# Kernel tuning notes

Measured on AMD Instinct MI355X. Metric: run time of the kernel, lower is better.

Reference implementation:

```python
import jax, jax.numpy as jnp
import numpy as np
from jax import lax

B, H, W, C = 2, 96, 96, 96
D_STATE, D_CONV, EXPAND = 16, 3, 2
D_INNER = EXPAND * C            # 192 (VSSBlock inner width)
DM = D_INNER                    # Mamba d_model; Mamba expand=1 -> mamba d_inner == DM
DT_RANK = -(-DM // 16)          # ceil(192/16) = 12


def setup_inputs() -> dict:
    key = jax.random.key(0)
    ks = jax.random.split(key, 12)
    s = lambda k, shp, sc=0.02: jax.random.normal(k, shp, jnp.float32) * sc
    return {
        "x": jax.random.normal(ks[0], (B, H, W, C), jnp.float32),
        "norm_w": jnp.ones((C,), jnp.float32),
        "norm_b": jnp.zeros((C,), jnp.float32),
        "in_proj_w": s(ks[1], (C, 2 * D_INNER)),
        "conv2d_w": s(ks[2], (D_INNER, 1, D_CONV, D_CONV), 0.1),   # depthwise OIHW
        "m_in_proj_w": s(ks[3], (DM, 2 * DM)),
        "m_conv1d_w": s(ks[4], (DM, 1, D_CONV), 0.1),              # depthwise causal OIL
        "m_conv1d_b": jnp.zeros((DM,), jnp.float32),
        "m_x_proj_w": s(ks[5], (DM, DT_RANK + 2 * D_STATE)),
        "m_dt_proj_w": s(ks[6], (DT_RANK, DM), 0.1),
        "m_dt_proj_b": s(ks[7], (DM,), 0.1),
        "m_A_log": jnp.log(jnp.broadcast_to(
            jnp.arange(1, D_STATE + 1, dtype=jnp.float32), (DM, D_STATE))),
        "m_D": jnp.ones((DM,), jnp.float32),
        "m_out_proj_w": s(ks[8], (DM, DM)),
        "out_proj_w": s(ks[9], (D_INNER, C)),
    }


def _layernorm(x, w, b, eps=1e-5):
    mu = x.mean(-1, keepdims=True)
    var = jnp.mean(jnp.square(x - mu), -1, keepdims=True)
    return (x - mu) * lax.rsqrt(var + eps) * w + b


def _selective_scan(u, delta, A, Bm, Cm, Dv):
    # u, delta: (B,L,D); A: (D,N); Bm, Cm: (B,L,N); Dv: (D,)
    dA = jnp.exp(jnp.einsum('bld,dn->bldn', delta, A))           # (B,L,D,N)
    dBu = jnp.einsum('bld,bln->bldn', delta * u, Bm)             # (B,L,D,N)

    def step(h, inp):
        dA_t, dBu_t, C_t = inp
        h = dA_t * h + dBu_t                                      # (B,D,N)
        y = jnp.einsum('bdn,bn->bd', h, C_t)
        return h, y

    h0 = jnp.zeros((u.shape[0], A.shape[0], A.shape[1]), u.dtype)
    xs = (dA.transpose(1, 0, 2, 3), dBu.transpose(1, 0, 2, 3), Cm.transpose(1, 0, 2))
    _, ys = lax.scan(step, h0, xs)
    return ys.transpose(1, 0, 2) + u * Dv                         # (B,L,D)


def _mamba(seq, m_in_proj_w, m_conv1d_w, m_conv1d_b, m_x_proj_w,
           m_dt_proj_w, m_dt_proj_b, m_A_log, m_D, m_out_proj_w):
    # seq: (B,L,DM)
    xm, z = jnp.split(seq @ m_in_proj_w, 2, axis=-1)
    # causal depthwise conv1d over L
    xc = lax.conv_general_dilated(
        jnp.transpose(xm, (0, 2, 1)), m_conv1d_w, (1,), [(D_CONV - 1, 0)],
        feature_group_count=DM, dimension_numbers=('NCH', 'OIH', 'NCH'))
    xm = jax.nn.silu(jnp.transpose(xc + m_conv1d_b[None, :, None], (0, 2, 1)))
    x_dbl = xm @ m_x_proj_w
    dt, Bm, Cm = jnp.split(x_dbl, [DT_RANK, DT_RANK + D_STATE], axis=-1)
    delta = jax.nn.softplus(dt @ m_dt_proj_w + m_dt_proj_b)
    A = -jnp.exp(m_A_log)
    y = _selective_scan(xm, delta, A, Bm, Cm, m_D)
    return (y * jax.nn.silu(z)) @ m_out_proj_w


def reference(x, norm_w, norm_b, in_proj_w, conv2d_w, m_in_proj_w, m_conv1d_w,
              m_conv1d_b, m_x_proj_w, m_dt_proj_w, m_dt_proj_b, m_A_log, m_D,
              m_out_proj_w, out_proj_w):
    Bsz, Hh, Ww, _ = x.shape
    xn = _layernorm(x, norm_w, norm_b)
    x_in, x_gate = jnp.split(xn @ in_proj_w, 2, axis=-1)          # (B,H,W,D_INNER) x2
    # depthwise 3x3 conv, 'same' padding
    xc = lax.conv_general_dilated(
        jnp.transpose(x_in, (0, 3, 1, 2)), conv2d_w, (1, 1), [(1, 1), (1, 1)],
        feature_group_count=D_INNER, dimension_numbers=('NCHW', 'OIHW', 'NCHW'))
    xc = jax.nn.silu(jnp.transpose(xc, (0, 2, 3, 1)))
    seq = xc.reshape(Bsz, Hh * Ww, D_INNER)
    y = _mamba(seq, m_in_proj_w, m_conv1d_w, m_conv1d_b, m_x_proj_w,
               m_dt_proj_w, m_dt_proj_b, m_A_log, m_D, m_out_proj_w)
    y = y.reshape(Bsz, Hh, Ww, D_INNER) * jax.nn.silu(x_gate)
    return x + y @ out_proj_w
```

## Files before the change

kernel.cpp:

```cpp
#include <hip/hip_runtime.h>

#define DEV_INLINE __device__ __forceinline__

constexpr int BATCH = 2;
constexpr int HH = 96, WW = 96, CC = 96;
constexpr int DI = 192;
constexpr int NS = 16;
constexpr int LSEQ = HH * WW;
constexpr int TT = BATCH * LSEQ;
constexpr int CHUNK = 32;
constexpr int NCHUNK = LSEQ / CHUNK;
constexpr int QDN = DI * NS;

typedef __attribute__((ext_vector_type(8))) short bf16x8;
typedef __attribute__((ext_vector_type(4))) float f32x4;

DEV_INLINE float silu_f(float x) { return x / (1.f + __expf(-x)); }
DEV_INLINE float softplus_f(float x) {
  return fmaxf(x, 0.f) + log1pf(__expf(-fabsf(x)));
}
DEV_INLINE ushort f2bf(float f) {
  union { float f; unsigned u; } c; c.f = f;
  unsigned u = c.u + 0x7FFF + ((c.u >> 16) & 1);
  return (ushort)(u >> 16);
}
DEV_INLINE float bf2f(ushort u) {
  union { unsigned u; float f; } c; c.u = ((unsigned)u) << 16; return c.f;
}

__global__ __launch_bounds__(256)
void castw_kernel(const float* __restrict__ w0, const float* __restrict__ w1,
                  const float* __restrict__ w2, const float* __restrict__ w3,
                  const float* __restrict__ wx, const float* __restrict__ wdt,
                  const float* __restrict__ wc1,
                  ushort* __restrict__ t0, ushort* __restrict__ t1,
                  ushort* __restrict__ t2, ushort* __restrict__ t3,
                  ushort* __restrict__ t4, ushort* __restrict__ t5,
                  float* __restrict__ cwT)
{
  int id = blockIdx.x * 256 + threadIdx.x;
  if (id < 36864) {
    int k = id % 96, n = id / 96;
    t0[id] = f2bf(w0[k * 384 + n]);
  } else if (id < 110592) {
    int j = id - 36864; int k = j % 192, n = j / 192;
    t1[j] = f2bf(w1[k * 384 + n]);
  } else if (id < 147456) {
    int j = id - 110592; int k = j % 192, n = j / 192;
    t2[j] = f2bf(w2[k * 192 + n]);
  } else if (id < 172032) {
    int j = id - 147456; int k = j % 192, n = j / 192;
    t3[j] = (n < 96) ? f2bf(w3[k * 96 + n]) : (ushort)0;
  } else if (id < 181248) {
    int j = id - 172032; int k = j % 192, n = j / 192;
    float v = 0.f;
    if (n < 16) v = wx[k * 44 + 12 + n];
    else if (n < 32) v = wx[k * 44 + 28 + (n - 16)];
    else if (n < 44) v = wx[k * 44 + (n - 32)];
    t4[j] = f2bf(v);
  } else if (id < 187392) {
    int j = id - 181248; int r = j % 32, d = j / 32;
    t5[j] = (r < 12) ? f2bf(wdt[r * 192 + d]) : (ushort)0;
  } else if (id < 187968) {
    int j = id - 187392; int k = j / 192, d = j % 192;
    cwT[j] = wc1[d * 3 + k];
  }
}

__global__ __launch_bounds__(256)
void ln_inproj_kernel(const float* __restrict__ x, const float* __restrict__ nw,
                      const float* __restrict__ nbias, const ushort* __restrict__ Wt0,
                      ushort* __restrict__ xz0)
{
  __shared__ ushort sA[128][104];
  const int tid = threadIdx.x;
  const int m0 = blockIdx.x * 128;
  const int n0 = blockIdx.y * 64;
  {
    const int tok = tid >> 1, h = tid & 1;
    const float* xr = x + (size_t)(m0 + tok) * 96 + h * 48;
    float v[48];
    float s = 0.f, ss = 0.f;
#pragma unroll
    for (int i = 0; i < 12; ++i) {
      float4 t4 = *(const float4*)(xr + i * 4);
      v[i*4+0] = t4.x; v[i*4+1] = t4.y; v[i*4+2] = t4.z; v[i*4+3] = t4.w;
      s += (t4.x + t4.y) + (t4.z + t4.w);
      ss += (t4.x*t4.x + t4.y*t4.y) + (t4.z*t4.z + t4.w*t4.w);
    }
    s += __shfl_xor(s, 1);
    ss += __shfl_xor(ss, 1);
    float mean = s * (1.f/96.f);
    float var = ss * (1.f/96.f) - mean*mean;
    float rstd = rsqrtf(var + 1e-5f);
    const float* wr = nw + h*48;
    const float* br = nbias + h*48;
#pragma unroll
    for (int i = 0; i < 12; ++i) {
      float4 w4 = *(const float4*)(wr + i*4);
      float4 b4 = *(const float4*)(br + i*4);
      unsigned p0 = (unsigned)f2bf((v[i*4+0]-mean)*rstd*w4.x + b4.x)
                  | ((unsigned)f2bf((v[i*4+1]-mean)*rstd*w4.y + b4.y) << 16);
      unsigned p1 = (unsigned)f2bf((v[i*4+2]-mean)*rstd*w4.z + b4.z)
                  | ((unsigned)f2bf((v[i*4+3]-mean)*rstd*w4.w + b4.w) << 16);
      unsigned* dst = (unsigned*)&sA[tok][h*48 + i*4];
      dst[0] = p0; dst[1] = p1;
    }
  }
  __syncthreads();

  const int wid = tid >> 6, lane = tid & 63;
  const int wm = wid >> 1, wn = wid & 1;
  const int l16 = lane & 15, quad = lane >> 4;
  const f32x4 z4 = {0.f, 0.f, 0.f, 0.f};
  f32x4 acc[4][2];
#pragma unroll
  for (int i = 0; i < 4; ++i)
#pragma unroll
    for (int j = 0; j < 2; ++j) acc[i][j] = z4;

#pragma unroll
  for (int k0 = 0; k0 < 96; k0 += 32) {
    bf16x8 xf[4], wf[2];
#pragma unroll
    for (int i = 0; i < 4; ++i)
      xf[i] = *(const bf16x8*)&sA[wm*64 + i*16 + l16][k0 + quad*8];
#pragma unroll
    for (int j = 0; j < 2; ++j)
      wf[j] = *(const bf16x8*)(Wt0 + (size_t)(n0 + wn*32 + j*16 + l16) * 96 + k0 + quad*8);
#pragma unroll
    for (int i = 0; i < 4; ++i)
#pragma unroll
      for (int j = 0; j < 2; ++j)
        acc[i][j] = __builtin_amdgcn_mfma_f32_16x16x32_bf16(wf[j], xf[i], acc[i][j], 0, 0, 0);
  }
#pragma unroll
  for (int i = 0; i < 4; ++i) {
    const int token = m0 + wm*64 + i*16 + l16;
#pragma unroll
    for (int j = 0; j < 2; ++j) {
      const int nb = n0 + wn*32 + j*16 + quad*4;
      ushort4 o;
      o.x = f2bf(acc[i][j][0]); o.y = f2bf(acc[i][j][1]);
      o.z = f2bf(acc[i][j][2]); o.w = f2bf(acc[i][j][3]);
      *(ushort4*)(xz0 + (size_t)token * 384 + nb) = o;
    }
  }
}

__global__ __launch_bounds__(256)
void mfma_gemm_kernel(const ushort* __restrict__ A, int lda,
                      const ushort* __restrict__ Bt, int ldb,
                      ushort* __restrict__ Cout, int ldc, int K)
{
  const int tid = threadIdx.x;
  const int wid = tid >> 6, lane = tid & 63;
  const int wm = wid >> 1, wn = wid & 1;
  const int m0 = blockIdx.x * 128 + wm * 64;
  const int n0 = blockIdx.y * 64 + wn * 32;
  const int l16 = lane & 15, quad = lane >> 4;

  f32x4 acc[4][2];
  const f32x4 z4 = {0.f, 0.f, 0.f, 0.f};
#pragma unroll
  for (int i = 0; i < 4; ++i)
#pragma unroll
    for (int j = 0; j < 2; ++j) acc[i][j] = z4;

  for (int k0 = 0; k0 < K; k0 += 32) {
    bf16x8 xf[4], wf[2];
#pragma unroll
    for (int i = 0; i < 4; ++i)
      xf[i] = *(const bf16x8*)(A + (size_t)(m0 + i * 16 + l16) * lda + k0 + quad * 8);
#pragma unroll
    for (int j = 0; j < 2; ++j)
      wf[j] = *(const bf16x8*)(Bt + (size_t)(n0 + j * 16 + l16) * ldb + k0 + quad * 8);
#pragma unroll
    for (int i = 0; i < 4; ++i)
#pragma unroll
      for (int j = 0; j < 2; ++j)
        acc[i][j] = __builtin_amdgcn_mfma_f32_16x16x32_bf16(wf[j], xf[i], acc[i][j], 0, 0, 0);
  }
#pragma unroll
  for (int i = 0; i < 4; ++i) {
    const int token = m0 + i * 16 + l16;
#pragma unroll
    for (int j = 0; j < 2; ++j) {
      const int nb = n0 + j * 16 + quad * 4;
      ushort4 o;
      o.x = f2bf(acc[i][j][0]); o.y = f2bf(acc[i][j][1]);
      o.z = f2bf(acc[i][j][2]); o.w = f2bf(acc[i][j][3]);
      *(ushort4*)(Cout + (size_t)token * ldc + nb) = o;
    }
  }
}

__global__ __launch_bounds__(256)
void conv2d_silu_kernel(const ushort* __restrict__ xz0, const float* __restrict__ w,
                        ushort* __restrict__ xc)
{
  __shared__ float ws[DI * 9];
  for (int i = threadIdx.x; i < DI * 9; i += 256) ws[i] = w[i];
  __syncthreads();
  int id = blockIdx.x * 256 + threadIdx.x;
  int dq = id % 48;
  int p  = id / 48;
  int j = p % WW;
  int i = (p / WW) % HH;
  int b = p / (WW * HH);
  int d = dq * 4;
  float a0 = 0.f, a1 = 0.f, a2 = 0.f, a3 = 0.f;
#pragma unroll
  for (int ki = 0; ki < 3; ++ki) {
    int ii = i + ki - 1;
    if (ii < 0 || ii >= HH) continue;
#pragma unroll
    for (int kj = 0; kj < 3; ++kj) {
      int jj = j + kj - 1;
      if (jj < 0 || jj >= WW) continue;
      const ushort4 v = *(const ushort4*)(xz0 + ((size_t)((b * HH + ii) * WW + jj)) * 384 + d);
      int wk = ki * 3 + kj;
      a0 = fmaf(bf2f(v.x), ws[(d + 0) * 9 + wk], a0);
      a1 = fmaf(bf2f(v.y), ws[(d + 1) * 9 + wk], a1);
      a2 = fmaf(bf2f(v.z), ws[(d + 2) * 9 + wk], a2);
      a3 = fmaf(bf2f(v.w), ws[(d + 3) * 9 + wk], a3);
    }
  }
  ushort4 o;
  o.x = f2bf(silu_f(a0)); o.y = f2bf(silu_f(a1));
  o.z = f2bf(silu_f(a2)); o.w = f2bf(silu_f(a3));
  *(ushort4*)(xc + (size_t)p * DI + d) = o;
}

__global__ __launch_bounds__(64)
void mprep_kernel(const ushort* __restrict__ xz1, const float* __restrict__ cwT,
                  const float* __restrict__ cb, const ushort* __restrict__ Wxt,
                  const ushort* __restrict__ Wdtt, const float* __restrict__ bdt,
                  ushort* __restrict__ xmb, float* __restrict__ xdbl_bc,
                  float* __restrict__ dlt)
{
  const int lane = threadIdx.x;
  const int l16 = lane & 15, quad = lane >> 4;
  const int t = blockIdx.x * 16 + l16;
  const int l = (t >= LSEQ) ? t - LSEQ : t;
  const f32x4 z4 = {0.f, 0.f, 0.f, 0.f};
  f32x4 accB = z4, accC = z4, accD = z4;

#pragma unroll
  for (int k0 = 0; k0 < 192; k0 += 32) {
    const int c = k0 + quad * 8;
    float4 b0 = *(const float4*)(cb + c);
    float4 b1 = *(const float4*)(cb + c + 4);
    float u[8] = {b0.x, b0.y, b0.z, b0.w, b1.x, b1.y, b1.z, b1.w};
#pragma unroll
    for (int k = 0; k < 3; ++k) {
      if (l + k - 2 < 0) continue;
      bf16x8 xv = *(const bf16x8*)(xz1 + (size_t)(t + k - 2) * 384 + c);
      float4 w0 = *(const float4*)(cwT + k * 192 + c);
      float4 w1 = *(const float4*)(cwT + k * 192 + c + 4);
      u[0] = fmaf(bf2f((ushort)xv[0]), w0.x, u[0]);
      u[1] = fmaf(bf2f((ushort)xv[1]), w0.y, u[1]);
      u[2] = fmaf(bf2f((ushort)xv[2]), w0.z, u[2]);
      u[3] = fmaf(bf2f((ushort)xv[3]), w0.w, u[3]);
      u[4] = fmaf(bf2f((ushort)xv[4]), w1.x, u[4]);
      u[5] = fmaf(bf2f((ushort)xv[5]), w1.y, u[5]);
      u[6] = fmaf(bf2f((ushort)xv[6]), w1.z, u[6]);
      u[7] = fmaf(bf2f((ushort)xv[7]), w1.w, u[7]);
    }
    bf16x8 uf;
#pragma unroll
    for (int jj = 0; jj < 8; ++jj) uf[jj] = (short)f2bf(silu_f(u[jj]));
    *(uint4*)(xmb + (size_t)t * DI + c) = *(uint4*)&uf;

    bf16x8 wB = *(const bf16x8*)(Wxt + (size_t)(l16) * 192 + c);
    bf16x8 wC = *(const bf16x8*)(Wxt + (size_t)(16 + l16) * 192 + c);
    bf16x8 wD = *(const bf16x8*)(Wxt + (size_t)(32 + l16) * 192 + c);
    accB = __builtin_amdgcn_mfma_f32_16x16x32_bf16(wB, uf, accB, 0, 0, 0);
    accC = __builtin_amdgcn_mfma_f32_16x16x32_bf16(wC, uf, accC, 0, 0, 0);
    accD = __builtin_amdgcn_mfma_f32_16x16x32_bf16(wD, uf, accD, 0, 0, 0);
  }
  *(float4*)(xdbl_bc + (size_t)t * 32 + quad * 4) =
      make_float4(accB[0], accB[1], accB[2], accB[3]);
  *(float4*)(xdbl_bc + (size_t)t * 32 + 16 + quad * 4) =
      make_float4(accC[0], accC[1], accC[2], accC[3]);

  bf16x8 dtf;
#pragma unroll
  for (int j = 0; j < 8; ++j) {
    int n = quad * 8 + j;
    int src = ((n >> 2) & 3) * 16 + l16;
    float tv = __shfl(accD[j & 3], src);
    dtf[j] = (short)((n < 16) ? f2bf(tv) : (ushort)0);
  }
  f32x4 acc2[12];
#pragma unroll
  for (int jj = 0; jj < 12; ++jj) {
    bf16x8 wf = *(const bf16x8*)(Wdtt + (size_t)(jj * 16 + l16) * 32 + quad * 8);
    acc2[jj] = __builtin_amdgcn_mfma_f32_16x16x32_bf16(wf, dtf, z4, 0, 0, 0);
  }
#pragma unroll
  for (int jj = 0; jj < 12; ++jj) {
    const int nb = jj * 16 + quad * 4;
    float4 b4 = *(const float4*)(bdt + nb);
    float4 dv;
    dv.x = softplus_f(acc2[jj][0] + b4.x);
    dv.y = softplus_f(acc2[jj][1] + b4.y);
    dv.z = softplus_f(acc2[jj][2] + b4.z);
    dv.w = softplus_f(acc2[jj][3] + b4.w);
    *(float4*)(dlt + (size_t)t * DI + nb) = dv;
  }
}

__global__ __launch_bounds__(192)
void scan1_kernel(const float* __restrict__ dlt, const ushort* __restrict__ xmb,
                  const float* __restrict__ xdbl_bc, const float* __restrict__ Alog,
                  float* __restrict__ P, float* __restrict__ E)
{
  const int d = threadIdx.x;
  const int g = blockIdx.x % NCHUNK;
  const int b = blockIdx.x / NCHUNK;
  const int t0 = b * LSEQ + g * CHUNK;
  float Av[16];
#pragma unroll
  for (int j = 0; j < 16; ++j) Av[j] = -__expf(Alog[d * 16 + j]);
  float e[16];
#pragma unroll
  for (int j = 0; j < 16; ++j) e[j] = 0.f;
  float sdl = 0.f;
#pragma unroll 2
  for (int l = 0; l < CHUNK; ++l) {
    const int t = t0 + l;
    float dl = dlt[(size_t)t * DI + d];
    float u  = bf2f(xmb[(size_t)t * DI + d]);
    const float4 B0 = *(const float4*)(xdbl_bc + (size_t)t * 32 + 0);
    const float4 B1 = *(const float4*)(xdbl_bc + (size_t)t * 32 + 4);
    const float4 B2 = *(const float4*)(xdbl_bc + (size_t)t * 32 + 8);
    const float4 B3 = *(const float4*)(xdbl_bc + (size_t)t * 32 + 12);
    const float Bv[16] = {B0.x, B0.y, B0.z, B0.w, B1.x, B1.y, B1.z, B1.w,
                          B2.x, B2.y, B2.z, B2.w, B3.x, B3.y, B3.z, B3.w};
    float du = dl * u;
    sdl += dl;
#pragma unroll
    for (int j = 0; j < 16; ++j) {
      float a = __expf(dl * Av[j]);
      e[j] = fmaf(a, e[j], du * Bv[j]);
    }
  }
  size_t base = ((size_t)(b * NCHUNK + g)) * QDN + d * 16;
#pragma unroll
  for (int j = 0; j < 16; ++j) {
    P[base + j] = __expf(Av[j] * sdl);
    E[base + j] = e[j];
  }
}

__global__ __launch_bounds__(256)
void scan2_kernel(const float* __restrict__ P, const float* __restrict__ E,
                  float* __restrict__ Hin)
{
  int id = blockIdx.x * 256 + threadIdx.x;
  int q = id % QDN;
  int b = id / QDN;
  float h = 0.f;
#pragma unroll 8
  for (int g = 0; g < NCHUNK; ++g) {
    size_t idx = ((size_t)(b * NCHUNK + g)) * QDN + q;
    Hin[idx] = h;
    h = fmaf(P[idx], h, E[idx]);
  }
}

__global__ __launch_bounds__(192)
void scan3_kernel(const float* __restrict__ dlt, const ushort* __restrict__ xmb,
                  const float* __restrict__ xdbl_bc, const float* __restrict__ Alog,
                  const float* __restrict__ Dv, const ushort* __restrict__ xz1,
                  const float* __restrict__ Hin, ushort* __restrict__ yout)
{
  const int d = threadIdx.x;
  const int g = blockIdx.x % NCHUNK;
  const int b = blockIdx.x / NCHUNK;
  const int t0 = b * LSEQ + g * CHUNK;
  float Av[16];
#pragma unroll
  for (int j = 0; j < 16; ++j) Av[j] = -__expf(Alog[d * 16 + j]);
  const float Dd = Dv[d];
  float h[16];
  {
    size_t hb = ((size_t)(b * NCHUNK + g)) * QDN + d * 16;
#pragma unroll
    for (int j = 0; j < 16; ++j) h[j] = Hin[hb + j];
  }
#pragma unroll 2
  for (int l = 0; l < CHUNK; ++l) {
    const int t = t0 + l;
    float dl = dlt[(size_t)t * DI + d];
    float u  = bf2f(xmb[(size_t)t * DI + d]);
    const float4 B0 = *(const float4*)(xdbl_bc + (size_t)t * 32 + 0);
    const float4 B1 = *(const float4*)(xdbl_bc + (size_t)t * 32 + 4);
    const float4 B2 = *(const float4*)(xdbl_bc + (size_t)t * 32 + 8);
    const float4 B3 = *(const float4*)(xdbl_bc + (size_t)t * 32 + 12);
    const float4 C0 = *(const float4*)(xdbl_bc + (size_t)t * 32 + 16);
    const float4 C1 = *(const float4*)(xdbl_bc + (size_t)t * 32 + 20);
    const float4 C2 = *(const float4*)(xdbl_bc + (size_t)t * 32 + 24);
    const float4 C3 = *(const float4*)(xdbl_bc + (size_t)t * 32 + 28);
    const float Bv[16] = {B0.x, B0.y, B0.z, B0.w, B1.x, B1.y, B1.z, B1.w,
                          B2.x, B2.y, B2.z, B2.w, B3.x, B3.y, B3.z, B3.w};
    const float Cv[16] = {C0.x, C0.y, C0.z, C0.w, C1.x, C1.y, C1.z, C1.w,
                          C2.x, C2.y, C2.z, C2.w, C3.x, C3.y, C3.z, C3.w};
    float du = dl * u;
    float y0 = 0.f, y1 = 0.f, y2 = 0.f, y3 = 0.f;
#pragma unroll
    for (int j = 0; j < 16; ++j) {
      float a = __expf(dl * Av[j]);
      h[j] = fmaf(a, h[j], du * Bv[j]);
      if ((j & 3) == 0) y0 = fmaf(h[j], Cv[j], y0);
      else if ((j & 3) == 1) y1 = fmaf(h[j], Cv[j], y1);
      else if ((j & 3) == 2) y2 = fmaf(h[j], Cv[j], y2);
      else y3 = fmaf(h[j], Cv[j], y3);
    }
    float y = (y0 + y1) + (y2 + y3) + u * Dd;
    float z = bf2f(xz1[(size_t)t * 384 + 192 + d]);
    yout[(size_t)t * DI + d] = f2bf(y * silu_f(z));
  }
}

__global__ __launch_bounds__(256)
void outproj_kernel(const ushort* __restrict__ yfin, const ushort* __restrict__ Wt2,
                    const ushort* __restrict__ xz0, const ushort* __restrict__ Wt3,
                    const float* __restrict__ x, float* __restrict__ out)
{
  __shared__ ushort yg_s[32][200];
  const int tid = threadIdx.x;
  const int wid = tid >> 6, lane = tid & 63;
  const int wm = wid >> 1, wn = wid & 1;
  const int l16 = lane & 15, quad = lane >> 4;
  const int m0 = blockIdx.x * 32;
  const f32x4 z4 = {0.f, 0.f, 0.f, 0.f};

  f32x4 acc[6];
#pragma unroll
  for (int j = 0; j < 6; ++j) acc[j] = z4;
  const int mt = m0 + wm * 16 + l16;
#pragma unroll
  for (int k0 = 0; k0 < 192; k0 += 32) {
    bf16x8 af = *(const bf16x8*)(yfin + (size_t)mt * 192 + k0 + quad * 8);
#pragma unroll
    for (int nj = 0; nj < 6; ++nj) {
      bf16x8 wf = *(const bf16x8*)(Wt2 + (size_t)(wn * 96 + nj * 16 + l16) * 192 + k0 + quad * 8);
      acc[nj] = __builtin_amdgcn_mfma_f32_16x16x32_bf16(wf, af, acc[nj], 0, 0, 0);
    }
  }
#pragma unroll
  for (int nj = 0; nj < 6; ++nj) {
    const int tok = wm * 16 + l16;
    const int nb = wn * 96 + nj * 16 + quad * 4;
    const ushort4 g4 = *(const ushort4*)(xz0 + (size_t)(m0 + tok) * 384 + 192 + nb);
    float v0 = acc[nj][0] * silu_f(bf2f(g4.x));
    float v1 = acc[nj][1] * silu_f(bf2f(g4.y));
    float v2 = acc[nj][2] * silu_f(bf2f(g4.z));
    float v3 = acc[nj][3] * silu_f(bf2f(g4.w));
    unsigned p0 = (unsigned)f2bf(v0) | ((unsigned)f2bf(v1) << 16);
    unsigned p1 = (unsigned)f2bf(v2) | ((unsigned)f2bf(v3) << 16);
    unsigned* dst = (unsigned*)&yg_s[tok][nb];
    dst[0] = p0; dst[1] = p1;
  }
  __syncthreads();

  f32x4 acc2[3];
#pragma unroll
  for (int j = 0; j < 3; ++j) acc2[j] = z4;
#pragma unroll
  for (int k0 = 0; k0 < 192; k0 += 32) {
    bf16x8 af = *(const bf16x8*)&yg_s[wm * 16 + l16][k0 + quad * 8];
#pragma unroll
    for (int nj = 0; nj < 3; ++nj) {
      bf16x8 wf = *(const bf16x8*)(Wt3 + (size_t)(wn * 48 + nj * 16 + l16) * 192 + k0 + quad * 8);
      acc2[nj] = __builtin_amdgcn_mfma_f32_16x16x32_bf16(wf, af, acc2[nj], 0, 0, 0);
    }
  }
#pragma unroll
  for (int nj = 0; nj < 3; ++nj) {
    const int tok = wm * 16 + l16;
    const int nb = wn * 48 + nj * 16 + quad * 4;
    const float4 r4 = *(const float4*)(x + (size_t)(m0 + tok) * 96 + nb);
    *(float4*)(out + (size_t)(m0 + tok) * 96 + nb) =
        make_float4(acc2[nj][0] + r4.x, acc2[nj][1] + r4.y,
                    acc2[nj][2] + r4.z, acc2[nj][3] + r4.w);
  }
}

extern "C" void kernel_launch(void* const* d_in, const int* in_sizes, int n_in,
                              void* d_out, int out_size, void* d_ws, size_t ws_size,
                              hipStream_t stream)
{
  const float* x         = (const float*)d_in[0];
  const float* norm_w    = (const float*)d_in[1];
  const float* norm_b    = (const float*)d_in[2];
  const float* in_proj_w = (const float*)d_in[3];
  const float* conv2d_w  = (const float*)d_in[4];
  const float* m_in_proj = (const float*)d_in[5];
  const float* m_c1d_w   = (const float*)d_in[6];
  const float* m_c1d_b   = (const float*)d_in[7];
  const float* m_x_proj  = (const float*)d_in[8];
  const float* m_dt_w    = (const float*)d_in[9];
  const float* m_dt_b    = (const float*)d_in[10];
  const float* m_A_log   = (const float*)d_in[11];
  const float* m_D       = (const float*)d_in[12];
  const float* m_out_w   = (const float*)d_in[13];
  const float* out_w     = (const float*)d_in[14];
  float* out = (float*)d_out;

  char* wp = (char*)d_ws;
  auto alloc = [&](size_t bytes) {
    char* r = wp; wp += (bytes + 255) & ~(size_t)255; return r;
  };
  ushort* Wt0    = (ushort*)alloc(36864 * 2);
  ushort* Wt1    = (ushort*)alloc(73728 * 2);
  ushort* Wt2    = (ushort*)alloc(36864 * 2);
  ushort* Wt3    = (ushort*)alloc(24576 * 2);
  ushort* Wxt    = (ushort*)alloc(9216 * 2);
  ushort* Wdtt   = (ushort*)alloc(6144 * 2);
  float*  cwT    = (float*)alloc(576 * 4);
  ushort* xz0    = (ushort*)alloc((size_t)TT * 384 * 2);
  ushort* xc_bf  = (ushort*)alloc((size_t)TT * 192 * 2);
  ushort* xz1    = (ushort*)alloc((size_t)TT * 384 * 2);
  ushort* xmb_bf = (ushort*)alloc((size_t)TT * 192 * 2);
  float*  xdbl_bc= (float*)alloc((size_t)TT * 32 * 4);
  float*  dlt    = (float*)alloc((size_t)TT * 192 * 4);
  float*  Pb     = (float*)alloc((size_t)BATCH * NCHUNK * QDN * 4);
  float*  Eb     = (float*)alloc((size_t)BATCH * NCHUNK * QDN * 4);
  float*  Hin    = (float*)alloc((size_t)BATCH * NCHUNK * QDN * 4);
  ushort* yfin   = (ushort*)alloc((size_t)TT * 192 * 2);

  castw_kernel<<<735, 256, 0, stream>>>(in_proj_w, m_in_proj, m_out_w, out_w,
                                        m_x_proj, m_dt_w, m_c1d_w,
                                        Wt0, Wt1, Wt2, Wt3, Wxt, Wdtt, cwT);
  ln_inproj_kernel<<<dim3(TT / 128, 6), 256, 0, stream>>>(x, norm_w, norm_b, Wt0, xz0);
  conv2d_silu_kernel<<<TT * 48 / 256, 256, 0, stream>>>(xz0, conv2d_w, xc_bf);
  mfma_gemm_kernel<<<dim3(TT / 128, 6), 256, 0, stream>>>(xc_bf, 192, Wt1, 192, xz1, 384, 192);
  mprep_kernel<<<TT / 16, 64, 0, stream>>>(xz1, cwT, m_c1d_b, Wxt, Wdtt, m_dt_b,
                                           xmb_bf, xdbl_bc, dlt);
  scan1_kernel<<<BATCH * NCHUNK, 192, 0, stream>>>(dlt, xmb_bf, xdbl_bc, m_A_log, Pb, Eb);
  scan2_kernel<<<BATCH * QDN / 256, 256, 0, stream>>>(Pb, Eb, Hin);
  scan3_kernel<<<BATCH * NCHUNK, 192, 0, stream>>>(dlt, xmb_bf, xdbl_bc, m_A_log, m_D, xz1, Hin, yfin);
  outproj_kernel<<<TT / 32, 256, 0, stream>>>(yfin, Wt2, xz0, Wt3, x, out);
}
```

Baseline: 261.8 us.

## Restructure Mamba scan pipeline with smaller chunks and hierarchical carry propagation

Halves the scan chunk length and replaces the serial inter-chunk carry pass with a three-level super-chunk scan (per-super-chunk reduce, carry pass, expand), so many more threads work in the carry phase. The fused per-token mprep kernel is split into separate conv1d, x_proj and dt_proj kernels. Delta is stored as bf16, B/C are staged in shared memory, P/E/Hin use a d-major layout for coalesced access, and the weight-cast kernel now reads its inputs coalesced. It adds more kernel launches and intermediate buffers, and bf16 delta reduces precision.

```diff
diff --git a/kernel.cpp b/kernel.cpp
--- a/kernel.cpp
+++ b/kernel.cpp
@@ -8,8 +8,9 @@
 constexpr int NS = 16;
 constexpr int LSEQ = HH * WW;
 constexpr int TT = BATCH * LSEQ;
-constexpr int CHUNK = 32;
+constexpr int CHUNK = 16;
 constexpr int NCHUNK = LSEQ / CHUNK;
+constexpr int SUP = 24, NSUP = NCHUNK / SUP;
 constexpr int QDN = DI * NS;
 
 typedef __attribute__((ext_vector_type(8))) short bf16x8;
@@ -40,30 +41,36 @@
 {
   int id = blockIdx.x * 256 + threadIdx.x;
   if (id < 36864) {
-    int k = id % 96, n = id / 96;
-    t0[id] = f2bf(w0[k * 384 + n]);
+    int k = id / 384, n = id % 384;
+    t0[n * 96 + k] = f2bf(w0[id]);
   } else if (id < 110592) {
-    int j = id - 36864; int k = j % 192, n = j / 192;
-    t1[j] = f2bf(w1[k * 384 + n]);
+    int j = id - 36864; int k = j / 384, n = j % 384;
+    t1[n * 192 + k] = f2bf(w1[j]);
   } else if (id < 147456) {
-    int j = id - 110592; int k = j % 192, n = j / 192;
-    t2[j] = f2bf(w2[k * 192 + n]);
+    int j = id - 110592; int k = j / 192, n = j % 192;
+    t2[n * 192 + k] = f2bf(w2[j]);
+  } else if (id < 165888) {
+    int j = id - 147456; int k = j / 96, n = j % 96;
+    t3[n * 192 + k] = f2bf(w3[j]);
   } else if (id < 172032) {
-    int j = id - 147456; int k = j % 192, n = j / 192;
-    t3[j] = (n < 96) ? f2bf(w3[k * 96 + n]) : (ushort)0;
+    int j = id - 165888;
+    t3[96 * 192 + j] = 0;
+  } else if (id < 180480) {
+    int j = id - 172032; int k = j / 44, c = j % 44;
+    int r = (c < 12) ? (32 + c) : (c < 28 ? (c - 12) : (16 + c - 28));
+    t4[r * 192 + k] = f2bf(wx[j]);
   } else if (id < 181248) {
-    int j = id - 172032; int k = j % 192, n = j / 192;
-    float v = 0.f;
-    if (n < 16) v = wx[k * 44 + 12 + n];
-    else if (n < 32) v = wx[k * 44 + 28 + (n - 16)];
-    else if (n < 44) v = wx[k * 44 + (n - 32)];
-    t4[j] = f2bf(v);
+    int j = id - 180480;
+    t4[44 * 192 + j] = 0;
+  } else if (id < 183552) {
+    int j = id - 181248; int r = j / 192, d = j % 192;
+    t5[d * 32 + r] = f2bf(wdt[j]);
   } else if (id < 187392) {
-    int j = id - 181248; int r = j % 32, d = j / 32;
-    t5[j] = (r < 12) ? f2bf(wdt[r * 192 + d]) : (ushort)0;
+    int j = id - 183552; int d = j / 20, r = 12 + j % 20;
+    t5[d * 32 + r] = 0;
   } else if (id < 187968) {
-    int j = id - 187392; int k = j / 192, d = j % 192;
-    cwT[j] = wc1[d * 3 + k];
+    int j = id - 187392; int d = j / 3, k = j % 3;
+    cwT[k * 192 + d] = wc1[j];
   }
 }
 
@@ -144,53 +151,6 @@
       o.x = f2bf(acc[i][j][0]); o.y = f2bf(acc[i][j][1]);
       o.z = f2bf(acc[i][j][2]); o.w = f2bf(acc[i][j][3]);
       *(ushort4*)(xz0 + (size_t)token * 384 + nb) = o;
-    }
-  }
-}
-
-__global__ __launch_bounds__(256)
-void mfma_gemm_kernel(const ushort* __restrict__ A, int lda,
-                      const ushort* __restrict__ Bt, int ldb,
-                      ushort* __restrict__ Cout, int ldc, int K)
-{
-  const int tid = threadIdx.x;
-  const int wid = tid >> 6, lane = tid & 63;
-  const int wm = wid >> 1, wn = wid & 1;
-  const int m0 = blockIdx.x * 128 + wm * 64;
-  const int n0 = blockIdx.y * 64 + wn * 32;
-  const int l16 = lane & 15, quad = lane >> 4;
-
-  f32x4 acc[4][2];
-  const f32x4 z4 = {0.f, 0.f, 0.f, 0.f};
-#pragma unroll
-  for (int i = 0; i < 4; ++i)
-#pragma unroll
-    for (int j = 0; j < 2; ++j) acc[i][j] = z4;
-
-  for (int k0 = 0; k0 < K; k0 += 32) {
-    bf16x8 xf[4], wf[2];
-#pragma unroll
-    for (int i = 0; i < 4; ++i)
-      xf[i] = *(const bf16x8*)(A + (size_t)(m0 + i * 16 + l16) * lda + k0 + quad * 8);
-#pragma unroll
-    for (int j = 0; j < 2; ++j)
-      wf[j] = *(const bf16x8*)(Bt + (size_t)(n0 + j * 16 + l16) * ldb + k0 + quad * 8);
-#pragma unroll
-    for (int i = 0; i < 4; ++i)
-#pragma unroll
-      for (int j = 0; j < 2; ++j)
-        acc[i][j] = __builtin_amdgcn_mfma_f32_16x16x32_bf16(wf[j], xf[i], acc[i][j], 0, 0, 0);
-  }
-#pragma unroll
-  for (int i = 0; i < 4; ++i) {
-    const int token = m0 + i * 16 + l16;
-#pragma unroll
-    for (int j = 0; j < 2; ++j) {
-      const int nb = n0 + j * 16 + quad * 4;
-      ushort4 o;
-      o.x = f2bf(acc[i][j][0]); o.y = f2bf(acc[i][j][1]);
-      o.z = f2bf(acc[i][j][2]); o.w = f2bf(acc[i][j][3]);
-      *(ushort4*)(Cout + (size_t)token * ldc + nb) = o;
     }
   }
 }
@@ -232,194 +192,279 @@
   *(ushort4*)(xc + (size_t)p * DI + d) = o;
 }
 
-__global__ __launch_bounds__(64)
-void mprep_kernel(const ushort* __restrict__ xz1, const float* __restrict__ cwT,
-                  const float* __restrict__ cb, const ushort* __restrict__ Wxt,
-                  const ushort* __restrict__ Wdtt, const float* __restrict__ bdt,
-                  ushort* __restrict__ xmb, float* __restrict__ xdbl_bc,
-                  float* __restrict__ dlt)
-{
-  const int lane = threadIdx.x;
+__global__ __launch_bounds__(256)
+void mfma_gemm_kernel(const ushort* __restrict__ A, int lda,
+                      const ushort* __restrict__ Bt, int ldb,
+                      ushort* __restrict__ Cout, int ldc, int K)
+{
+  const int tid = threadIdx.x;
+  const int wid = tid >> 6, lane = tid & 63;
+  const int wm = wid >> 1, wn = wid & 1;
+  const int m0 = blockIdx.x * 128 + wm * 64;
+  const int n0 = blockIdx.y * 64 + wn * 32;
   const int l16 = lane & 15, quad = lane >> 4;
-  const int t = blockIdx.x * 16 + l16;
-  const int l = (t >= LSEQ) ? t - LSEQ : t;
+
+  f32x4 acc[4][2];
   const f32x4 z4 = {0.f, 0.f, 0.f, 0.f};
-  f32x4 accB = z4, accC = z4, accD = z4;
-
+#pragma unroll
+  for (int i = 0; i < 4; ++i)
+#pragma unroll
+    for (int j = 0; j < 2; ++j) acc[i][j] = z4;
+
+  for (int k0 = 0; k0 < K; k0 += 32) {
+    bf16x8 xf[4], wf[2];
+#pragma unroll
+    for (int i = 0; i < 4; ++i)
+      xf[i] = *(const bf16x8*)(A + (size_t)(m0 + i * 16 + l16) * lda + k0 + quad * 8);
+#pragma unroll
+    for (int j = 0; j < 2; ++j)
+      wf[j] = *(const bf16x8*)(Bt + (size_t)(n0 + j * 16 + l16) * ldb + k0 + quad * 8);
+#pragma unroll
+    for (int i = 0; i < 4; ++i)
+#pragma unroll
+      for (int j = 0; j < 2; ++j)
+        acc[i][j] = __builtin_amdgcn_mfma_f32_16x16x32_bf16(wf[j], xf[i], acc[i][j], 0, 0, 0);
+  }
+#pragma unroll
+  for (int i = 0; i < 4; ++i) {
+    const int token = m0 + i * 16 + l16;
+#pragma unroll
+    for (int j = 0; j < 2; ++j) {
+      const int nb = n0 + j * 16 + quad * 4;
+      ushort4 o;
+      o.x = f2bf(acc[i][j][0]); o.y = f2bf(acc[i][j][1]);
+      o.z = f2bf(acc[i][j][2]); o.w = f2bf(acc[i][j][3]);
+      *(ushort4*)(Cout + (size_t)token * ldc + nb) = o;
+    }
+  }
+}
+
+__global__ __launch_bounds__(256)
+void conv1d_silu_kernel(const ushort* __restrict__ xz1, const float* __restrict__ cwT,
+                        const float* __restrict__ bias, ushort* __restrict__ xm)
+{
+  int id = blockIdx.x * 256 + threadIdx.x;
+  int dq = id % 48;
+  int t  = id / 48;
+  int l  = t % LSEQ;
+  int d  = dq * 4;
+  float4 b4 = *(const float4*)(bias + d);
+  float a0 = b4.x, a1 = b4.y, a2 = b4.z, a3 = b4.w;
+#pragma unroll
+  for (int k = 0; k < 3; ++k) {
+    if (l + k - 2 < 0) continue;
+    const ushort4 v = *(const ushort4*)(xz1 + (size_t)(t + k - 2) * 384 + d);
+    const float4 w4 = *(const float4*)(cwT + k * 192 + d);
+    a0 = fmaf(bf2f(v.x), w4.x, a0);
+    a1 = fmaf(bf2f(v.y), w4.y, a1);
+    a2 = fmaf(bf2f(v.z), w4.z, a2);
+    a3 = fmaf(bf2f(v.w), w4.w, a3);
+  }
+  ushort4 o;
+  o.x = f2bf(silu_f(a0)); o.y = f2bf(silu_f(a1));
+  o.z = f2bf(silu_f(a2)); o.w = f2bf(silu_f(a3));
+  *(ushort4*)(xm + (size_t)t * DI + d) = o;
+}
+
+__global__ __launch_bounds__(256)
+void xproj_kernel(const ushort* __restrict__ xmb, const ushort* __restrict__ Wxt,
+                  float* __restrict__ xdbl_bc, ushort* __restrict__ dtpad)
+{
+  const int w = blockIdx.x * 4 + (threadIdx.x >> 6);
+  const int lane = threadIdx.x & 63;
+  const int s = w / 3, tile = w % 3;
+  const int l16 = lane & 15, quad = lane >> 4;
+  const int token = s * 16 + l16;
+
+  f32x4 acc = {0.f, 0.f, 0.f, 0.f};
 #pragma unroll
   for (int k0 = 0; k0 < 192; k0 += 32) {
-    const int c = k0 + quad * 8;
-    float4 b0 = *(const float4*)(cb + c);
-    float4 b1 = *(const float4*)(cb + c + 4);
-    float u[8] = {b0.x, b0.y, b0.z, b0.w, b1.x, b1.y, b1.z, b1.w};
-#pragma unroll
-    for (int k = 0; k < 3; ++k) {
-      if (l + k - 2 < 0) continue;
-      bf16x8 xv = *(const bf16x8*)(xz1 + (size_t)(t + k - 2) * 384 + c);
-      float4 w0 = *(const float4*)(cwT + k * 192 + c);
-      float4 w1 = *(const float4*)(cwT + k * 192 + c + 4);
-      u[0] = fmaf(bf2f((ushort)xv[0]), w0.x, u[0]);
-      u[1] = fmaf(bf2f((ushort)xv[1]), w0.y, u[1]);
-      u[2] = fmaf(bf2f((ushort)xv[2]), w0.z, u[2]);
-      u[3] = fmaf(bf2f((ushort)xv[3]), w0.w, u[3]);
-      u[4] = fmaf(bf2f((ushort)xv[4]), w1.x, u[4]);
-      u[5] = fmaf(bf2f((ushort)xv[5]), w1.y, u[5]);
-      u[6] = fmaf(bf2f((ushort)xv[6]), w1.z, u[6]);
-      u[7] = fmaf(bf2f((ushort)xv[7]), w1.w, u[7]);
-    }
-    bf16x8 uf;
-#pragma unroll
-    for (int jj = 0; jj < 8; ++jj) uf[jj] = (short)f2bf(silu_f(u[jj]));
-    *(uint4*)(xmb + (size_t)t * DI + c) = *(uint4*)&uf;
-
-    bf16x8 wB = *(const bf16x8*)(Wxt + (size_t)(l16) * 192 + c);
-    bf16x8 wC = *(const bf16x8*)(Wxt + (size_t)(16 + l16) * 192 + c);
-    bf16x8 wD = *(const bf16x8*)(Wxt + (size_t)(32 + l16) * 192 + c);
-    accB = __builtin_amdgcn_mfma_f32_16x16x32_bf16(wB, uf, accB, 0, 0, 0);
-    accC = __builtin_amdgcn_mfma_f32_16x16x32_bf16(wC, uf, accC, 0, 0, 0);
-    accD = __builtin_amdgcn_mfma_f32_16x16x32_bf16(wD, uf, accD, 0, 0, 0);
-  }
-  *(float4*)(xdbl_bc + (size_t)t * 32 + quad * 4) =
-      make_float4(accB[0], accB[1], accB[2], accB[3]);
-  *(float4*)(xdbl_bc + (size_t)t * 32 + 16 + quad * 4) =
-      make_float4(accC[0], accC[1], accC[2], accC[3]);
-
-  bf16x8 dtf;
-#pragma unroll
-  for (int j = 0; j < 8; ++j) {
-    int n = quad * 8 + j;
-    int src = ((n >> 2) & 3) * 16 + l16;
-    float tv = __shfl(accD[j & 3], src);
-    dtf[j] = (short)((n < 16) ? f2bf(tv) : (ushort)0);
-  }
-  f32x4 acc2[12];
-#pragma unroll
-  for (int jj = 0; jj < 12; ++jj) {
-    bf16x8 wf = *(const bf16x8*)(Wdtt + (size_t)(jj * 16 + l16) * 32 + quad * 8);
-    acc2[jj] = __builtin_amdgcn_mfma_f32_16x16x32_bf16(wf, dtf, z4, 0, 0, 0);
-  }
-#pragma unroll
-  for (int jj = 0; jj < 12; ++jj) {
-    const int nb = jj * 16 + quad * 4;
-    float4 b4 = *(const float4*)(bdt + nb);
-    float4 dv;
-    dv.x = softplus_f(acc2[jj][0] + b4.x);
-    dv.y = softplus_f(acc2[jj][1] + b4.y);
-    dv.z = softplus_f(acc2[jj][2] + b4.z);
-    dv.w = softplus_f(acc2[jj][3] + b4.w);
-    *(float4*)(dlt + (size_t)t * DI + nb) = dv;
+    bf16x8 xf = *(const bf16x8*)(xmb + (size_t)token * DI + k0 + quad * 8);
+    bf16x8 wf = *(const bf16x8*)(Wxt + (size_t)(tile * 16 + l16) * 192 + k0 + quad * 8);
+    acc = __builtin_amdgcn_mfma_f32_16x16x32_bf16(wf, xf, acc, 0, 0, 0);
+  }
+  if (tile < 2) {
+    *(float4*)(xdbl_bc + (size_t)token * 32 + tile * 16 + quad * 4) =
+        make_float4(acc[0], acc[1], acc[2], acc[3]);
+  } else {
+    ushort4 o;
+    o.x = f2bf(acc[0]); o.y = f2bf(acc[1]); o.z = f2bf(acc[2]); o.w = f2bf(acc[3]);
+    *(ushort4*)(dtpad + (size_t)token * 32 + quad * 4) = o;
+    *(ushort4*)(dtpad + (size_t)token * 32 + 16 + quad * 4) = make_ushort4(0, 0, 0, 0);
+  }
+}
+
+__global__ __launch_bounds__(256)
+void dtproj_kernel(const ushort* __restrict__ dtpad, const ushort* __restrict__ Wdtt,
+                   const float* __restrict__ bdt, ushort* __restrict__ dlt)
+{
+  const int w = blockIdx.x * 4 + (threadIdx.x >> 6);
+  const int lane = threadIdx.x & 63;
+  const int s = w / 3, cg = w % 3;
+  const int l16 = lane & 15, quad = lane >> 4;
+  const int token = s * 16 + l16;
+  const f32x4 z4 = {0.f, 0.f, 0.f, 0.f};
+
+  bf16x8 dtf = *(const bf16x8*)(dtpad + (size_t)token * 32 + quad * 8);
+  f32x4 acc[4];
+#pragma unroll
+  for (int jj = 0; jj < 4; ++jj) {
+    bf16x8 wf = *(const bf16x8*)(Wdtt + (size_t)(cg * 64 + jj * 16 + l16) * 32 + quad * 8);
+    acc[jj] = __builtin_amdgcn_mfma_f32_16x16x32_bf16(wf, dtf, z4, 0, 0, 0);
+  }
+#pragma unroll
+  for (int jj = 0; jj < 4; ++jj) {
+    const int nb = cg * 64 + jj * 16 + quad * 4;
+    const float4 b4 = *(const float4*)(bdt + nb);
+    ushort4 o;
+    o.x = f2bf(softplus_f(acc[jj][0] + b4.x));
+    o.y = f2bf(softplus_f(acc[jj][1] + b4.y));
+    o.z = f2bf(softplus_f(acc[jj][2] + b4.z));
+    o.w = f2bf(softplus_f(acc[jj][3] + b4.w));
+    *(ushort4*)(dlt + (size_t)token * DI + nb) = o;
   }
 }
 
 __global__ __launch_bounds__(192)
-void scan1_kernel(const float* __restrict__ dlt, const ushort* __restrict__ xmb,
-                  const float* __restrict__ xdbl_bc, const float* __restrict__ Alog,
+void scan1_kernel(const ushort* __restrict__ dlt, const ushort* __restrict__ xmb,
+                  const float* __restrict__ bc, const float* __restrict__ Alog,
                   float* __restrict__ P, float* __restrict__ E)
 {
+  __shared__ float sB[CHUNK][16];
   const int d = threadIdx.x;
   const int g = blockIdx.x % NCHUNK;
   const int b = blockIdx.x / NCHUNK;
   const int t0 = b * LSEQ + g * CHUNK;
+  for (int i = threadIdx.x; i < CHUNK * 16; i += 192) {
+    int l = i >> 4, j = i & 15;
+    sB[l][j] = bc[(size_t)(t0 + l) * 32 + j];
+  }
   float Av[16];
 #pragma unroll
   for (int j = 0; j < 16; ++j) Av[j] = -__expf(Alog[d * 16 + j]);
+  __syncthreads();
   float e[16];
 #pragma unroll
   for (int j = 0; j < 16; ++j) e[j] = 0.f;
   float sdl = 0.f;
-#pragma unroll 2
+#pragma unroll 4
   for (int l = 0; l < CHUNK; ++l) {
     const int t = t0 + l;
-    float dl = dlt[(size_t)t * DI + d];
+    float dl = bf2f(dlt[(size_t)t * DI + d]);
     float u  = bf2f(xmb[(size_t)t * DI + d]);
-    const float4 B0 = *(const float4*)(xdbl_bc + (size_t)t * 32 + 0);
-    const float4 B1 = *(const float4*)(xdbl_bc + (size_t)t * 32 + 4);
-    const float4 B2 = *(const float4*)(xdbl_bc + (size_t)t * 32 + 8);
-    const float4 B3 = *(const float4*)(xdbl_bc + (size_t)t * 32 + 12);
-    const float Bv[16] = {B0.x, B0.y, B0.z, B0.w, B1.x, B1.y, B1.z, B1.w,
-                          B2.x, B2.y, B2.z, B2.w, B3.x, B3.y, B3.z, B3.w};
     float du = dl * u;
     sdl += dl;
 #pragma unroll
     for (int j = 0; j < 16; ++j) {
       float a = __expf(dl * Av[j]);
-      e[j] = fmaf(a, e[j], du * Bv[j]);
-    }
-  }
-  size_t base = ((size_t)(b * NCHUNK + g)) * QDN + d * 16;
+      e[j] = fmaf(a, e[j], du * sB[l][j]);
+    }
+  }
+  size_t base = ((size_t)(b * NCHUNK + g)) * QDN + d;
 #pragma unroll
   for (int j = 0; j < 16; ++j) {
-    P[base + j] = __expf(Av[j] * sdl);
-    E[base + j] = e[j];
-  }
-}
-
-__global__ __launch_bounds__(256)
-void scan2_kernel(const float* __restrict__ P, const float* __restrict__ E,
-                  float* __restrict__ Hin)
+    P[base + j * 192] = __expf(Av[j] * sdl);
+    E[base + j * 192] = e[j];
+  }
+}
+
+__global__ __launch_bounds__(256)
+void scan2a_kernel(const float* __restrict__ P, const float* __restrict__ E,
+                   float* __restrict__ SP, float* __restrict__ SE)
+{
+  int id = blockIdx.x * 256 + threadIdx.x;
+  int q = id % QDN;
+  int s = (id / QDN) % NSUP;
+  int b = id / (QDN * NSUP);
+  float cp = 1.f, ce = 0.f;
+#pragma unroll 6
+  for (int c = 0; c < SUP; ++c) {
+    size_t idx = ((size_t)(b * NCHUNK + s * SUP + c)) * QDN + q;
+    float p = P[idx], e = E[idx];
+    ce = fmaf(p, ce, e);
+    cp *= p;
+  }
+  SP[id] = cp; SE[id] = ce;
+}
+
+__global__ __launch_bounds__(256)
+void scan2b_kernel(const float* __restrict__ SP, const float* __restrict__ SE,
+                   float* __restrict__ Hsup)
 {
   int id = blockIdx.x * 256 + threadIdx.x;
   int q = id % QDN;
   int b = id / QDN;
-  float h = 0.f;
-#pragma unroll 8
-  for (int g = 0; g < NCHUNK; ++g) {
-    size_t idx = ((size_t)(b * NCHUNK + g)) * QDN + q;
+  float carry = 0.f;
+#pragma unroll
+  for (int s = 0; s < NSUP; ++s) {
+    size_t idx = ((size_t)(b * NSUP + s)) * QDN + q;
+    Hsup[idx] = carry;
+    carry = fmaf(SP[idx], carry, SE[idx]);
+  }
+}
+
+__global__ __launch_bounds__(256)
+void scan2c_kernel(const float* __restrict__ P, const float* __restrict__ E,
+                   const float* __restrict__ Hsup, float* __restrict__ Hin)
+{
+  int id = blockIdx.x * 256 + threadIdx.x;
+  int q = id % QDN;
+  int s = (id / QDN) % NSUP;
+  int b = id / (QDN * NSUP);
+  float h = Hsup[id];
+#pragma unroll 6
+  for (int c = 0; c < SUP; ++c) {
+    size_t idx = ((size_t)(b * NCHUNK + s * SUP + c)) * QDN + q;
     Hin[idx] = h;
     h = fmaf(P[idx], h, E[idx]);
   }
 }
 
 __global__ __launch_bounds__(192)
-void scan3_kernel(const float* __restrict__ dlt, const ushort* __restrict__ xmb,
-                  const float* __restrict__ xdbl_bc, const float* __restrict__ Alog,
+void scan3_kernel(const ushort* __restrict__ dlt, const ushort* __restrict__ xmb,
+                  const float* __restrict__ bc, const float* __restrict__ Alog,
                   const float* __restrict__ Dv, const ushort* __restrict__ xz1,
                   const float* __restrict__ Hin, ushort* __restrict__ yout)
 {
+  __shared__ float sBC[CHUNK][32];
   const int d = threadIdx.x;
   const int g = blockIdx.x % NCHUNK;
   const int b = blockIdx.x / NCHUNK;
   const int t0 = b * LSEQ + g * CHUNK;
+  for (int i = threadIdx.x; i < CHUNK * 32; i += 192) {
+    int l = i >> 5, j = i & 31;
+    sBC[l][j] = bc[(size_t)(t0 + l) * 32 + j];
+  }
   float Av[16];
 #pragma unroll
   for (int j = 0; j < 16; ++j) Av[j] = -__expf(Alog[d * 16 + j]);
   const float Dd = Dv[d];
   float h[16];
   {
-    size_t hb = ((size_t)(b * NCHUNK + g)) * QDN + d * 16;
-#pragma unroll
-    for (int j = 0; j < 16; ++j) h[j] = Hin[hb + j];
-  }
-#pragma unroll 2
+    size_t hb = ((size_t)(b * NCHUNK + g)) * QDN + d;
+#pragma unroll
+    for (int j = 0; j < 16; ++j) h[j] = Hin[hb + j * 192];
+  }
+  __syncthreads();
+#pragma unroll 4
   for (int l = 0; l < CHUNK; ++l) {
     const int t = t0 + l;
-    float dl = dlt[(size_t)t * DI + d];
+    float dl = bf2f(dlt[(size_t)t * DI + d]);
     float u  = bf2f(xmb[(size_t)t * DI + d]);
-    const float4 B0 = *(const float4*)(xdbl_bc + (size_t)t * 32 + 0);
-    const float4 B1 = *(const float4*)(xdbl_bc + (size_t)t * 32 + 4);
-    const float4 B2 = *(const float4*)(xdbl_bc + (size_t)t * 32 + 8);
-    const float4 B3 = *(const float4*)(xdbl_bc + (size_t)t * 32 + 12);
-    const float4 C0 = *(const float4*)(xdbl_bc + (size_t)t * 32 + 16);
-    const float4 C1 = *(const float4*)(xdbl_bc + (size_t)t * 32 + 20);
-    const float4 C2 = *(const float4*)(xdbl_bc + (size_t)t * 32 + 24);
-    const float4 C3 = *(const float4*)(xdbl_bc + (size_t)t * 32 + 28);
-    const float Bv[16] = {B0.x, B0.y, B0.z, B0.w, B1.x, B1.y, B1.z, B1.w,
-                          B2.x, B2.y, B2.z, B2.w, B3.x, B3.y, B3.z, B3.w};
-    const float Cv[16] = {C0.x, C0.y, C0.z, C0.w, C1.x, C1.y, C1.z, C1.w,
-                          C2.x, C2.y, C2.z, C2.w, C3.x, C3.y, C3.z, C3.w};
+    float z  = bf2f(xz1[(size_t)t * 384 + 192 + d]);
     float du = dl * u;
     float y0 = 0.f, y1 = 0.f, y2 = 0.f, y3 = 0.f;
 #pragma unroll
     for (int j = 0; j < 16; ++j) {
       float a = __expf(dl * Av[j]);
-      h[j] = fmaf(a, h[j], du * Bv[j]);
-      if ((j & 3) == 0) y0 = fmaf(h[j], Cv[j], y0);
-      else if ((j & 3) == 1) y1 = fmaf(h[j], Cv[j], y1);
-      else if ((j & 3) == 2) y2 = fmaf(h[j], Cv[j], y2);
-      else y3 = fmaf(h[j], Cv[j], y3);
+      h[j] = fmaf(a, h[j], du * sBC[l][j]);
+      float hc = h[j] * sBC[l][16 + j];
+      if ((j & 3) == 0) y0 += hc;
+      else if ((j & 3) == 1) y1 += hc;
+      else if ((j & 3) == 2) y2 += hc;
+      else y3 += hc;
     }
     float y = (y0 + y1) + (y2 + y3) + u * Dd;
-    float z = bf2f(xz1[(size_t)t * 384 + 192 + d]);
     yout[(size_t)t * DI + d] = f2bf(y * silu_f(z));
   }
 }
@@ -429,7 +474,7 @@
                     const ushort* __restrict__ xz0, const ushort* __restrict__ Wt3,
                     const float* __restrict__ x, float* __restrict__ out)
 {
-  __shared__ ushort yg_s[32][200];
+  __shared__ ushort yg_s[32][204];
   const int tid = threadIdx.x;
   const int wid = tid >> 6, lane = tid & 63;
   const int wm = wid >> 1, wn = wid & 1;
@@ -520,28 +565,35 @@
   ushort* Wt3    = (ushort*)alloc(24576 * 2);
   ushort* Wxt    = (ushort*)alloc(9216 * 2);
   ushort* Wdtt   = (ushort*)alloc(6144 * 2);
-  float*  cwT    = (float*)alloc(576 * 4);
+  float*  cw1T   = (float*)alloc(576 * 4);
   ushort* xz0    = (ushort*)alloc((size_t)TT * 384 * 2);
   ushort* xc_bf  = (ushort*)alloc((size_t)TT * 192 * 2);
   ushort* xz1    = (ushort*)alloc((size_t)TT * 384 * 2);
   ushort* xmb_bf = (ushort*)alloc((size_t)TT * 192 * 2);
-  float*  xdbl_bc= (float*)alloc((size_t)TT * 32 * 4);
-  float*  dlt    = (float*)alloc((size_t)TT * 192 * 4);
-  float*  Pb     = (float*)alloc((size_t)BATCH * NCHUNK * QDN * 4);
-  float*  Eb     = (float*)alloc((size_t)BATCH * NCHUNK * QDN * 4);
+  ushort* dtpad  = (ushort*)alloc((size_t)TT * 32 * 2);
+  float*  bc     = (float*)alloc((size_t)TT * 32 * 4);
+  ushort* dlt    = (ushort*)alloc((size_t)TT * 192 * 2);
+  float*  P      = (float*)alloc((size_t)BATCH * NCHUNK * QDN * 4);
+  float*  E      = (float*)alloc((size_t)BATCH * NCHUNK * QDN * 4);
+  float*  SP     = (float*)alloc((size_t)BATCH * NSUP * QDN * 4);
+  float*  SE     = (float*)alloc((size_t)BATCH * NSUP * QDN * 4);
+  float*  Hsup   = (float*)alloc((size_t)BATCH * NSUP * QDN * 4);
   float*  Hin    = (float*)alloc((size_t)BATCH * NCHUNK * QDN * 4);
   ushort* yfin   = (ushort*)alloc((size_t)TT * 192 * 2);
 
   castw_kernel<<<735, 256, 0, stream>>>(in_proj_w, m_in_proj, m_out_w, out_w,
                                         m_x_proj, m_dt_w, m_c1d_w,
-                                        Wt0, Wt1, Wt2, Wt3, Wxt, Wdtt, cwT);
+                                        Wt0, Wt1, Wt2, Wt3, Wxt, Wdtt, cw1T);
   ln_inproj_kernel<<<dim3(TT / 128, 6), 256, 0, stream>>>(x, norm_w, norm_b, Wt0, xz0);
   conv2d_silu_kernel<<<TT * 48 / 256, 256, 0, stream>>>(xz0, conv2d_w, xc_bf);
   mfma_gemm_kernel<<<dim3(TT / 128, 6), 256, 0, stream>>>(xc_bf, 192, Wt1, 192, xz1, 384, 192);
-  mprep_kernel<<<TT / 16, 64, 0, stream>>>(xz1, cwT, m_c1d_b, Wxt, Wdtt, m_dt_b,
-                                           xmb_bf, xdbl_bc, dlt);
-  scan1_kernel<<<BATCH * NCHUNK, 192, 0, stream>>>(dlt, xmb_bf, xdbl_bc, m_A_log, Pb, Eb);
-  scan2_kernel<<<BATCH * QDN / 256, 256, 0, stream>>>(Pb, Eb, Hin);
-  scan3_kernel<<<BATCH * NCHUNK, 192, 0, stream>>>(dlt, xmb_bf, xdbl_bc, m_A_log, m_D, xz1, Hin, yfin);
+  conv1d_silu_kernel<<<TT * 48 / 256, 256, 0, stream>>>(xz1, cw1T, m_c1d_b, xmb_bf);
+  xproj_kernel<<<TT / 16 * 3 / 4, 256, 0, stream>>>(xmb_bf, Wxt, bc, dtpad);
+  dtproj_kernel<<<TT / 16 * 3 / 4, 256, 0, stream>>>(dtpad, Wdtt, m_dt_b, dlt);
+  scan1_kernel<<<BATCH * NCHUNK, 192, 0, stream>>>(dlt, xmb_bf, bc, m_A_log, P, E);
+  scan2a_kernel<<<BATCH * NSUP * QDN / 256, 256, 0, stream>>>(P, E, SP, SE);
+  scan2b_kernel<<<BATCH * QDN / 256, 256, 0, stream>>>(SP, SE, Hsup);
+  scan2c_kernel<<<BATCH * NSUP * QDN / 256, 256, 0, stream>>>(P, E, Hsup, Hin);
+  scan3_kernel<<<BATCH * NCHUNK, 192, 0, stream>>>(dlt, xmb_bf, bc, m_A_log, m_D, xz1, Hin, yfin);
   outproj_kernel<<<TT / 32, 256, 0, stream>>>(yfin, Wt2, xz0, Wt3, x, out);
 }
```

Result: faster. 239.5 us (-8.5%).
